# Performance work log

Hardware: AMD Instinct MI355X
Metric: run time of the kernel (lower is better)

Reference implementation:

```python
import jax, jax.numpy as jnp
import numpy as np

N_NODES = 80000
N_EDGES = 1280000
N_FEAT = 4
HIDDEN = 64
N_CLASSES = 2
N_GRAPHS = 64
BN_EPS = 1e-5


def setup_inputs() -> dict:
    key = jax.random.key(0)
    ks = jax.random.split(key, 16)
    x = jax.random.normal(ks[0], (N_NODES, N_FEAT), dtype=jnp.float32)
    edge_index = jax.random.randint(ks[1], (2, N_EDGES), 0, N_NODES, dtype=jnp.int64)
    batch = jnp.sort(jax.random.randint(ks[2], (N_NODES,), 0, N_GRAPHS, dtype=jnp.int64))

    def lin_w(k, fan_in, fan_out):
        bound = 1.0 / np.sqrt(fan_in)
        return jax.random.uniform(k, (fan_in, fan_out), jnp.float32, -bound, bound)

    inp = {
        "x": x, "edge_index": edge_index, "batch": batch,
        # BatchNorm1d (eval mode: running stats)
        "bn_gamma": jnp.ones((N_FEAT,), jnp.float32),
        "bn_beta": jnp.zeros((N_FEAT,), jnp.float32),
        "bn_mean": jnp.zeros((N_FEAT,), jnp.float32),
        "bn_var": jnp.ones((N_FEAT,), jnp.float32),
        # GraphConv layers: out = agg @ W_rel + b_rel + x @ W_root
        "W1_rel": lin_w(ks[3], N_FEAT, HIDDEN), "b1_rel": jnp.zeros((HIDDEN,), jnp.float32),
        "W1_root": lin_w(ks[4], N_FEAT, HIDDEN),
        "W2_rel": lin_w(ks[5], HIDDEN, HIDDEN), "b2_rel": jnp.zeros((HIDDEN,), jnp.float32),
        "W2_root": lin_w(ks[6], HIDDEN, HIDDEN),
        "W3_rel": lin_w(ks[7], HIDDEN, HIDDEN), "b3_rel": jnp.zeros((HIDDEN,), jnp.float32),
        "W3_root": lin_w(ks[8], HIDDEN, HIDDEN),
        "lin_W": lin_w(ks[9], HIDDEN, N_CLASSES),
        "lin_b": jnp.zeros((N_CLASSES,), jnp.float32),
    }
    return inp


def _graph_conv(x, src, dst, W_rel, b_rel, W_root):
    # PyG GraphConv: x_i' = W_root x_i + W_rel * sum_{j in N(i)} x_j + b_rel
    agg = jax.ops.segment_sum(x[src], dst, num_segments=N_NODES)  # [N, C_in]
    return agg @ W_rel + b_rel + x @ W_root


def reference(x, edge_index, batch,
              bn_gamma, bn_beta, bn_mean, bn_var,
              W1_rel, b1_rel, W1_root,
              W2_rel, b2_rel, W2_root,
              W3_rel, b3_rel, W3_root,
              lin_W, lin_b):
    src, dst = edge_index[0], edge_index[1]
    # BatchNorm1d, eval mode (running stats); dropout is a no-op in eval.
    h = (x - bn_mean) * (bn_gamma * jax.lax.rsqrt(bn_var + BN_EPS)) + bn_beta
    h = jax.nn.relu(_graph_conv(h, src, dst, W1_rel, b1_rel, W1_root))
    h = jax.nn.relu(_graph_conv(h, src, dst, W2_rel, b2_rel, W2_root))
    h = _graph_conv(h, src, dst, W3_rel, b3_rel, W3_root)
    # global mean pool over graphs
    sums = jax.ops.segment_sum(h, batch, num_segments=N_GRAPHS)        # [G, H]
    cnts = jax.ops.segment_sum(jnp.ones((h.shape[0],), h.dtype), batch,
                               num_segments=N_GRAPHS)                  # [G]
    pooled = sums / jnp.maximum(cnts, 1.0)[:, None]
    return pooled @ lin_W + lin_b  # [G, num_classes]
```

## Files before the change

kernel.cpp:

```cpp
#include <hip/hip_runtime.h>
#include <hip/hip_bf16.h>

#define N_NODES 80000
#define N_EDGES 1280000
#define N_FEAT 4
#define HIDDEN 64
#define N_GRAPHS 64
#define BN_EPS 1e-5f

#define NBUCK 313
#define BCAP 8000
#define EPT 16

typedef unsigned short ushort_t;
typedef __attribute__((ext_vector_type(8))) short bf16x8;
typedef __attribute__((ext_vector_type(4))) float f32x4;

__device__ __forceinline__ float bf2f(ushort_t v) {
    return __uint_as_float(((unsigned)v) << 16);
}
__device__ __forceinline__ ushort_t f2bf(float f) {
    unsigned u = __float_as_uint(f);
    u += 0x7FFFu + ((u >> 16) & 1u);
    return (ushort_t)(u >> 16);
}

__global__ void wprep_kernel(const float* __restrict__ W2_rel,
                             const float* __restrict__ W2_root,
                             const float* __restrict__ W3_rel,
                             const float* __restrict__ W3_root,
                             ushort_t* __restrict__ WcatT2,
                             ushort_t* __restrict__ WcatT3,
                             int* __restrict__ bcursor,
                             float* __restrict__ pool,
                             float* __restrict__ cnt) {
    int i = blockIdx.x * blockDim.x + threadIdx.x;
    int which = i >= 64 * 128;
    int j = i & (64 * 128 - 1);
    int n = j >> 7, k = j & 127;
    const float* Wr = which ? W3_rel : W2_rel;
    const float* Wo = which ? W3_root : W2_root;
    ushort_t* Wc = which ? WcatT3 : WcatT2;
    float w = (k < 64) ? Wr[k * 64 + n] : Wo[(k - 64) * 64 + n];
    Wc[j] = f2bf(w);
    if (i < 4096) pool[i] = 0.f;
    else if (i < 4160) cnt[i - 4096] = 0.f;
    else if (i < 4160 + NBUCK) bcursor[i - 4160] = 0;
}

__global__ __launch_bounds__(256) void bucket_kernel(
        const int* __restrict__ src, const int* __restrict__ dst,
        int2* __restrict__ pairs, int* __restrict__ bcursor) {
    __shared__ int hist[NBUCK];
    __shared__ int base[NBUCK];
    for (int i = threadIdx.x; i < NBUCK; i += 256) hist[i] = 0;
    __syncthreads();
    const int e0 = blockIdx.x * (256 * EPT) + threadIdx.x;
    int d[EPT], r[EPT];
#pragma unroll
    for (int k = 0; k < EPT; ++k) {
        int e = e0 + k * 256;
        if (e < N_EDGES) {
            d[k] = dst[e];
            r[k] = atomicAdd(&hist[d[k] >> 8], 1);
        }
    }
    __syncthreads();
    for (int i = threadIdx.x; i < NBUCK; i += 256) {
        int c = hist[i];
        base[i] = c ? atomicAdd(&bcursor[i], c) : 0;
    }
    __syncthreads();
#pragma unroll
    for (int k = 0; k < EPT; ++k) {
        int e = e0 + k * 256;
        if (e < N_EDGES) {
            int b = d[k] >> 8;
            int pos = base[b] + r[k];
            if (pos < BCAP) pairs[(size_t)b * BCAP + pos] = make_int2(src[e], d[k]);
        }
    }
}

__global__ __launch_bounds__(512) void bucket_scan_kernel(
        const int* __restrict__ bcursor, int* __restrict__ bbase,
        int* __restrict__ rowstart) {
    __shared__ int s[512];
    const int t = threadIdx.x;
    int v = (t < NBUCK) ? min(bcursor[t], BCAP) : 0;
    s[t] = v;
    __syncthreads();
    for (int off = 1; off < 512; off <<= 1) {
        int u = (t >= off) ? s[t - off] : 0;
        __syncthreads();
        s[t] += u;
        __syncthreads();
    }
    if (t < NBUCK) bbase[t] = s[t] - v;
    if (t == NBUCK - 1) rowstart[N_NODES] = s[t];
}

__global__ __launch_bounds__(256) void csr_build_kernel(
        const int2* __restrict__ pairs, const int* __restrict__ bcursor,
        const int* __restrict__ bbase,
        int* __restrict__ rowstart, int* __restrict__ csr) {
    __shared__ int degl[256];
    __shared__ int pref[256];
    __shared__ int curs[256];
    const int b = blockIdx.x;
    const int t = threadIdx.x;
    const int cnt = min(bcursor[b], BCAP);
    const int base = bbase[b];
    degl[t] = 0;
    __syncthreads();
    const int2* pb = pairs + (size_t)b * BCAP;
    for (int i = t; i < cnt; i += 256) {
        atomicAdd(&degl[pb[i].y & 255], 1);
    }
    __syncthreads();
    int v = degl[t];
    pref[t] = v;
    __syncthreads();
    for (int off = 1; off < 256; off <<= 1) {
        int u = (t >= off) ? pref[t - off] : 0;
        __syncthreads();
        pref[t] += u;
        __syncthreads();
    }
    int excl = pref[t] - v;
    int node = b * 256 + t;
    if (node < N_NODES) rowstart[node] = base + excl;
    curs[t] = excl;
    __syncthreads();
    for (int i = t; i < cnt; i += 256) {
        int2 p = pb[i];
        int pos = atomicAdd(&curs[p.y & 255], 1);
        csr[base + pos] = p.x;
    }
}

__global__ __launch_bounds__(1024) void layer1_kernel(
        const float* __restrict__ x, ushort_t* __restrict__ h1,
        const int* __restrict__ rowstart, const int* __restrict__ csr,
        const float* __restrict__ Wrel, const float* __restrict__ Wroot,
        const float* __restrict__ b,
        const float* __restrict__ gamma, const float* __restrict__ beta,
        const float* __restrict__ mean, const float* __restrict__ var) {
    const int lane = threadIdx.x & 63;
    const int wid = threadIdx.x >> 6;
    float scale[4], shift[4];
#pragma unroll
    for (int k = 0; k < 4; ++k) {
        float sc = gamma[k] * rsqrtf(var[k] + BN_EPS);
        scale[k] = sc;
        shift[k] = beta[k] - mean[k] * sc;
    }
    float wrel2[4], wroot2[4];
    float crel = 0.f, croot = 0.f;
#pragma unroll
    for (int k = 0; k < 4; ++k) {
        float wr = Wrel[k * 64 + lane], wo = Wroot[k * 64 + lane];
        wrel2[k] = scale[k] * wr;  crel += shift[k] * wr;
        wroot2[k] = scale[k] * wo; croot += shift[k] * wo;
    }
    const float bj = b[lane] + croot;
    const int sub = lane >> 2;
    const int f = lane & 3;
    const int nW = gridDim.x * 16;
    for (int n0 = blockIdx.x * 16 + wid; n0 < N_NODES; n0 += nW) {
        const int node = __builtin_amdgcn_readfirstlane(n0);
        const int e0 = rowstart[node], e1 = rowstart[node + 1];
        const float deg = (float)(e1 - e0);
        float part = 0.f;
        for (int e = e0 + sub; e < e1; e += 16) {
            int s = csr[e];
            part += x[s * 4 + f];
        }
        part += __shfl_xor(part, 4);
        part += __shfl_xor(part, 8);
        part += __shfl_xor(part, 16);
        part += __shfl_xor(part, 32);
        float a0 = __shfl(part, 0), a1 = __shfl(part, 1);
        float a2 = __shfl(part, 2), a3 = __shfl(part, 3);
        float x0 = x[node * 4 + 0], x1 = x[node * 4 + 1];
        float x2 = x[node * 4 + 2], x3 = x[node * 4 + 3];
        float out = bj + deg * crel
                  + a0 * wrel2[0] + a1 * wrel2[1] + a2 * wrel2[2] + a3 * wrel2[3]
                  + x0 * wroot2[0] + x1 * wroot2[1] + x2 * wroot2[2] + x3 * wroot2[3];
        h1[(size_t)node * 64 + lane] = f2bf(fmaxf(out, 0.f));
    }
}

__global__ __launch_bounds__(256) void gather_kernel(
        const ushort_t* __restrict__ hin, ushort_t* __restrict__ Gagg,
        const int* __restrict__ rowstart, const int* __restrict__ csr) {
    const int lane = threadIdx.x & 63;
    const int node = __builtin_amdgcn_readfirstlane(blockIdx.x * 4 + (threadIdx.x >> 6));
    const int e0 = rowstart[node], e1 = rowstart[node + 1];
    float a0 = 0.f, a1 = 0.f, a2 = 0.f, a3 = 0.f;
    float a4 = 0.f, a5 = 0.f, a6 = 0.f, a7 = 0.f;
    int e = e0;
    for (; e + 16 <= e1; e += 16) {
        int idx = csr[e + (lane & 15)];
        int s0 = __builtin_amdgcn_readlane(idx, 0);
        int s1 = __builtin_amdgcn_readlane(idx, 1);
        int s2 = __builtin_amdgcn_readlane(idx, 2);
        int s3 = __builtin_amdgcn_readlane(idx, 3);
        int s4 = __builtin_amdgcn_readlane(idx, 4);
        int s5 = __builtin_amdgcn_readlane(idx, 5);
        int s6 = __builtin_amdgcn_readlane(idx, 6);
        int s7 = __builtin_amdgcn_readlane(idx, 7);
        int s8 = __builtin_amdgcn_readlane(idx, 8);
        int s9 = __builtin_amdgcn_readlane(idx, 9);
        int s10 = __builtin_amdgcn_readlane(idx, 10);
        int s11 = __builtin_amdgcn_readlane(idx, 11);
        int s12 = __builtin_amdgcn_readlane(idx, 12);
        int s13 = __builtin_amdgcn_readlane(idx, 13);
        int s14 = __builtin_amdgcn_readlane(idx, 14);
        int s15 = __builtin_amdgcn_readlane(idx, 15);
        ushort_t v0 = hin[(size_t)s0 * 64 + lane];
        ushort_t v1 = hin[(size_t)s1 * 64 + lane];
        ushort_t v2 = hin[(size_t)s2 * 64 + lane];
        ushort_t v3 = hin[(size_t)s3 * 64 + lane];
        ushort_t v4 = hin[(size_t)s4 * 64 + lane];
        ushort_t v5 = hin[(size_t)s5 * 64 + lane];
        ushort_t v6 = hin[(size_t)s6 * 64 + lane];
        ushort_t v7 = hin[(size_t)s7 * 64 + lane];
        ushort_t v8 = hin[(size_t)s8 * 64 + lane];
        ushort_t v9 = hin[(size_t)s9 * 64 + lane];
        ushort_t v10 = hin[(size_t)s10 * 64 + lane];
        ushort_t v11 = hin[(size_t)s11 * 64 + lane];
        ushort_t v12 = hin[(size_t)s12 * 64 + lane];
        ushort_t v13 = hin[(size_t)s13 * 64 + lane];
        ushort_t v14 = hin[(size_t)s14 * 64 + lane];
        ushort_t v15 = hin[(size_t)s15 * 64 + lane];
        a0 += bf2f(v0) + bf2f(v8);
        a1 += bf2f(v1) + bf2f(v9);
        a2 += bf2f(v2) + bf2f(v10);
        a3 += bf2f(v3) + bf2f(v11);
        a4 += bf2f(v4) + bf2f(v12);
        a5 += bf2f(v5) + bf2f(v13);
        a6 += bf2f(v6) + bf2f(v14);
        a7 += bf2f(v7) + bf2f(v15);
    }
    if (e + 8 <= e1) {
        int idx = csr[e + (lane & 7)];
        int s0 = __builtin_amdgcn_readlane(idx, 0);
        int s1 = __builtin_amdgcn_readlane(idx, 1);
        int s2 = __builtin_amdgcn_readlane(idx, 2);
        int s3 = __builtin_amdgcn_readlane(idx, 3);
        int s4 = __builtin_amdgcn_readlane(idx, 4);
        int s5 = __builtin_amdgcn_readlane(idx, 5);
        int s6 = __builtin_amdgcn_readlane(idx, 6);
        int s7 = __builtin_amdgcn_readlane(idx, 7);
        ushort_t v0 = hin[(size_t)s0 * 64 + lane];
        ushort_t v1 = hin[(size_t)s1 * 64 + lane];
        ushort_t v2 = hin[(size_t)s2 * 64 + lane];
        ushort_t v3 = hin[(size_t)s3 * 64 + lane];
        ushort_t v4 = hin[(size_t)s4 * 64 + lane];
        ushort_t v5 = hin[(size_t)s5 * 64 + lane];
        ushort_t v6 = hin[(size_t)s6 * 64 + lane];
        ushort_t v7 = hin[(size_t)s7 * 64 + lane];
        a0 += bf2f(v0); a1 += bf2f(v1); a2 += bf2f(v2); a3 += bf2f(v3);
        a4 += bf2f(v4); a5 += bf2f(v5); a6 += bf2f(v6); a7 += bf2f(v7);
        e += 8;
    }
    if (e + 4 <= e1) {
        int idx = csr[e + (lane & 3)];
        int s0 = __builtin_amdgcn_readlane(idx, 0);
        int s1 = __builtin_amdgcn_readlane(idx, 1);
        int s2 = __builtin_amdgcn_readlane(idx, 2);
        int s3 = __builtin_amdgcn_readlane(idx, 3);
        ushort_t v0 = hin[(size_t)s0 * 64 + lane];
        ushort_t v1 = hin[(size_t)s1 * 64 + lane];
        ushort_t v2 = hin[(size_t)s2 * 64 + lane];
        ushort_t v3 = hin[(size_t)s3 * 64 + lane];
        a0 += bf2f(v0); a1 += bf2f(v1); a2 += bf2f(v2); a3 += bf2f(v3);
        e += 4;
    }
    for (; e < e1; ++e) {
        int s = __builtin_amdgcn_readfirstlane(csr[e]);
        a0 += bf2f(hin[(size_t)s * 64 + lane]);
    }
    float agg = ((a0 + a1) + (a2 + a3)) + ((a4 + a5) + (a6 + a7));
    Gagg[(size_t)node * 64 + lane] = f2bf(agg);
}

__global__ __launch_bounds__(256) void gemm_kernel(
        const ushort_t* __restrict__ Gagg, const ushort_t* __restrict__ hin,
        ushort_t* __restrict__ hout,
        const ushort_t* __restrict__ WcatT, const float* __restrict__ b,
        int relu) {
    const int lane = threadIdx.x & 63;
    const int col = lane & 15;
    const int grp = lane >> 4;

    bf16x8 bf[4][4];
#pragma unroll
    for (int kt = 0; kt < 4; ++kt)
#pragma unroll
        for (int nt = 0; nt < 4; ++nt)
            bf[kt][nt] = *(const bf16x8*)&WcatT[(nt * 16 + col) * 128 + kt * 32 + grp * 8];

    float bj[4];
#pragma unroll
    for (int nt = 0; nt < 4; ++nt) bj[nt] = b[nt * 16 + col];

    const int tile = blockIdx.x * 4 + (threadIdx.x >> 6);
    if (tile >= N_NODES / 16) return;
    const int node0 = tile * 16;

    const ushort_t* ga = Gagg + (size_t)(node0 + col) * 64 + grp * 8;
    const ushort_t* ha = hin + (size_t)(node0 + col) * 64 + grp * 8;
    f32x4 acc0 = {0.f, 0.f, 0.f, 0.f};
    f32x4 acc1 = {0.f, 0.f, 0.f, 0.f};
    f32x4 acc2 = {0.f, 0.f, 0.f, 0.f};
    f32x4 acc3 = {0.f, 0.f, 0.f, 0.f};
#pragma unroll
    for (int kt = 0; kt < 4; ++kt) {
        bf16x8 a = (kt < 2) ? *(const bf16x8*)(ga + kt * 32)
                            : *(const bf16x8*)(ha + (kt - 2) * 32);
        acc0 = __builtin_amdgcn_mfma_f32_16x16x32_bf16(a, bf[kt][0], acc0, 0, 0, 0);
        acc1 = __builtin_amdgcn_mfma_f32_16x16x32_bf16(a, bf[kt][1], acc1, 0, 0, 0);
        acc2 = __builtin_amdgcn_mfma_f32_16x16x32_bf16(a, bf[kt][2], acc2, 0, 0, 0);
        acc3 = __builtin_amdgcn_mfma_f32_16x16x32_bf16(a, bf[kt][3], acc3, 0, 0, 0);
    }

#pragma unroll
    for (int nt = 0; nt < 4; ++nt) {
        f32x4 acc = (nt == 0) ? acc0 : (nt == 1) ? acc1 : (nt == 2) ? acc2 : acc3;
        const int c = nt * 16 + col;
#pragma unroll
        for (int r = 0; r < 4; ++r) {
            int row = grp * 4 + r;
            float v = acc[r] + bj[nt];
            if (relu) v = fmaxf(v, 0.f);
            hout[(size_t)(node0 + row) * 64 + c] = f2bf(v);
        }
    }
}

__global__ void pool_kernel(const ushort_t* __restrict__ h3, const int* __restrict__ batch,
                            float* __restrict__ pool, float* __restrict__ cnt) {
    const int lane = threadIdx.x & 63;
    const int gw = (blockIdx.x * blockDim.x + threadIdx.x) >> 6;
    const int nW = (gridDim.x * blockDim.x) >> 6;
    const int chunk = (N_NODES + nW - 1) / nW;
    int n0 = gw * chunk;
    int n1 = n0 + chunk; if (n1 > N_NODES) n1 = N_NODES;
    if (n0 >= N_NODES) return;
    float acc = 0.f;
    int cur = batch[n0];
    int cl = 0;
#define POOL_FLUSH() do { atomicAdd(&pool[cur * 64 + lane], acc); \
        if (lane == 0) atomicAdd(&cnt[cur], (float)cl); acc = 0.f; cl = 0; } while (0)
    int n = n0;
    for (; n + 8 <= n1; n += 8) {
        float v0 = bf2f(h3[(size_t)(n + 0) * 64 + lane]);
        float v1 = bf2f(h3[(size_t)(n + 1) * 64 + lane]);
        float v2 = bf2f(h3[(size_t)(n + 2) * 64 + lane]);
        float v3 = bf2f(h3[(size_t)(n + 3) * 64 + lane]);
        float v4 = bf2f(h3[(size_t)(n + 4) * 64 + lane]);
        float v5 = bf2f(h3[(size_t)(n + 5) * 64 + lane]);
        float v6 = bf2f(h3[(size_t)(n + 6) * 64 + lane]);
        float v7 = bf2f(h3[(size_t)(n + 7) * 64 + lane]);
        int g0 = batch[n + 0], g1 = batch[n + 1], g2 = batch[n + 2], g3 = batch[n + 3];
        int g4 = batch[n + 4], g5 = batch[n + 5], g6 = batch[n + 6], g7 = batch[n + 7];
        if (g0 != cur) { POOL_FLUSH(); cur = g0; } acc += v0; cl++;
        if (g1 != cur) { POOL_FLUSH(); cur = g1; } acc += v1; cl++;
        if (g2 != cur) { POOL_FLUSH(); cur = g2; } acc += v2; cl++;
        if (g3 != cur) { POOL_FLUSH(); cur = g3; } acc += v3; cl++;
        if (g4 != cur) { POOL_FLUSH(); cur = g4; } acc += v4; cl++;
        if (g5 != cur) { POOL_FLUSH(); cur = g5; } acc += v5; cl++;
        if (g6 != cur) { POOL_FLUSH(); cur = g6; } acc += v6; cl++;
        if (g7 != cur) { POOL_FLUSH(); cur = g7; } acc += v7; cl++;
    }
    for (; n < n1; ++n) {
        int g = batch[n];
        if (g != cur) { POOL_FLUSH(); cur = g; }
        acc += bf2f(h3[(size_t)n * 64 + lane]);
        cl++;
    }
    atomicAdd(&pool[cur * 64 + lane], acc);
    if (lane == 0) atomicAdd(&cnt[cur], (float)cl);
#undef POOL_FLUSH
}

__global__ void head_kernel(const float* __restrict__ pool, const float* __restrict__ cnt,
                            const float* __restrict__ linW, const float* __restrict__ linb,
                            float* __restrict__ out) {
    int g = threadIdx.x >> 1;
    int c = threadIdx.x & 1;
    if (g < N_GRAPHS) {
        float inv = 1.0f / fmaxf(cnt[g], 1.0f);
        float acc = linb[c];
        for (int j = 0; j < 64; ++j) acc += pool[g * 64 + j] * inv * linW[j * 2 + c];
        out[g * 2 + c] = acc;
    }
}

extern "C" void kernel_launch(void* const* d_in, const int* in_sizes, int n_in,
                              void* d_out, int out_size, void* d_ws, size_t ws_size,
                              hipStream_t stream) {
    const float* x = (const float*)d_in[0];
    const int* edge_index = (const int*)d_in[1];
    const int* batch = (const int*)d_in[2];
    const float* bn_gamma = (const float*)d_in[3];
    const float* bn_beta = (const float*)d_in[4];
    const float* bn_mean = (const float*)d_in[5];
    const float* bn_var = (const float*)d_in[6];
    const float* W1_rel = (const float*)d_in[7];
    const float* b1_rel = (const float*)d_in[8];
    const float* W1_root = (const float*)d_in[9];
    const float* W2_rel = (const float*)d_in[10];
    const float* b2_rel = (const float*)d_in[11];
    const float* W2_root = (const float*)d_in[12];
    const float* W3_rel = (const float*)d_in[13];
    const float* b3_rel = (const float*)d_in[14];
    const float* W3_root = (const float*)d_in[15];
    const float* lin_W = (const float*)d_in[16];
    const float* lin_b = (const float*)d_in[17];
    float* out = (float*)d_out;

    const int* e_src = edge_index;
    const int* e_dst = edge_index + N_EDGES;

    ushort_t* h1 = (ushort_t*)d_ws;
    ushort_t* h2 = h1 + 5120000;
    float* pool = (float*)(h2 + 5120000);
    float* cnt = pool + 4096;
    int* bcursor = (int*)(cnt + 64);
    int* bbase = bcursor + 320;
    int* rowstart = bbase + 320;
    int* csr = rowstart + 80016;
    ushort_t* WcatT2 = (ushort_t*)(csr + 1280000);
    ushort_t* WcatT3 = WcatT2 + 8192;
    ushort_t* Gagg = (ushort_t*)(WcatT3 + 8192 + 16);
    int2* pairs = (int2*)h1;
    ushort_t* h3 = h1;

    wprep_kernel<<<64, 256, 0, stream>>>(W2_rel, W2_root, W3_rel, W3_root,
                                         WcatT2, WcatT3, bcursor, pool, cnt);

    bucket_kernel<<<(N_EDGES + 256 * EPT - 1) / (256 * EPT), 256, 0, stream>>>(
        e_src, e_dst, pairs, bcursor);
    bucket_scan_kernel<<<1, 512, 0, stream>>>(bcursor, bbase, rowstart);
    csr_build_kernel<<<NBUCK, 256, 0, stream>>>(pairs, bcursor, bbase, rowstart, csr);

    layer1_kernel<<<512, 1024, 0, stream>>>(x, h1, rowstart, csr, W1_rel, W1_root,
                                            b1_rel, bn_gamma, bn_beta, bn_mean, bn_var);

    gather_kernel<<<N_NODES / 4, 256, 0, stream>>>(h1, Gagg, rowstart, csr);
    gemm_kernel<<<N_NODES / 64, 256, 0, stream>>>(Gagg, h1, h2, WcatT2, b2_rel, 1);

    gather_kernel<<<N_NODES / 4, 256, 0, stream>>>(h2, Gagg, rowstart, csr);
    gemm_kernel<<<N_NODES / 64, 256, 0, stream>>>(Gagg, h2, h3, WcatT3, b3_rel, 0);

    pool_kernel<<<256, 256, 0, stream>>>(h3, batch, pool, cnt);
    head_kernel<<<1, 128, 0, stream>>>(pool, cnt, lin_W, lin_b, out);
}
```

Before: 175.9 us.

## Pack edge pairs to 32 bits, fold bucket scan into CSR build, fuse pool+head

Edge pairs are packed into one 32-bit word (17-bit source, 8-bit local destination) instead of an int2, halving the bucket write and read traffic. The separate single-block bucket scan is removed: each CSR-build block recomputes its own base with a block reduction over the preceding bucket counts. The pooling and head kernels are merged, with the last block to finish (tracked by an atomic counter) computing the final linear layer. Together this drops two kernel launches at the cost of redundant prefix sums and a global completion counter.

Measured after the change: 182.9 us. 4.0% more time.

```diff
diff --git a/kernel.cpp b/kernel.cpp
--- a/kernel.cpp
+++ b/kernel.cpp
@@ -33,7 +33,8 @@
                              ushort_t* __restrict__ WcatT3,
                              int* __restrict__ bcursor,
                              float* __restrict__ pool,
-                             float* __restrict__ cnt) {
+                             float* __restrict__ cnt,
+                             int* __restrict__ done) {
     int i = blockIdx.x * blockDim.x + threadIdx.x;
     int which = i >= 64 * 128;
     int j = i & (64 * 128 - 1);
@@ -46,11 +47,12 @@
     if (i < 4096) pool[i] = 0.f;
     else if (i < 4160) cnt[i - 4096] = 0.f;
     else if (i < 4160 + NBUCK) bcursor[i - 4160] = 0;
+    else if (i == 4160 + NBUCK) *done = 0;
 }
 
 __global__ __launch_bounds__(256) void bucket_kernel(
         const int* __restrict__ src, const int* __restrict__ dst,
-        int2* __restrict__ pairs, int* __restrict__ bcursor) {
+        unsigned* __restrict__ pairs, int* __restrict__ bcursor) {
     __shared__ int hist[NBUCK];
     __shared__ int base[NBUCK];
     for (int i = threadIdx.x; i < NBUCK; i += 256) hist[i] = 0;
@@ -77,45 +79,37 @@
         if (e < N_EDGES) {
             int b = d[k] >> 8;
             int pos = base[b] + r[k];
-            if (pos < BCAP) pairs[(size_t)b * BCAP + pos] = make_int2(src[e], d[k]);
-        }
-    }
-}
-
-__global__ __launch_bounds__(512) void bucket_scan_kernel(
-        const int* __restrict__ bcursor, int* __restrict__ bbase,
-        int* __restrict__ rowstart) {
-    __shared__ int s[512];
-    const int t = threadIdx.x;
-    int v = (t < NBUCK) ? min(bcursor[t], BCAP) : 0;
-    s[t] = v;
-    __syncthreads();
-    for (int off = 1; off < 512; off <<= 1) {
-        int u = (t >= off) ? s[t - off] : 0;
-        __syncthreads();
-        s[t] += u;
-        __syncthreads();
-    }
-    if (t < NBUCK) bbase[t] = s[t] - v;
-    if (t == NBUCK - 1) rowstart[N_NODES] = s[t];
+            if (pos < BCAP)
+                pairs[(size_t)b * BCAP + pos] =
+                    (unsigned)src[e] | (((unsigned)d[k] & 255u) << 17);
+        }
+    }
 }
 
 __global__ __launch_bounds__(256) void csr_build_kernel(
-        const int2* __restrict__ pairs, const int* __restrict__ bcursor,
-        const int* __restrict__ bbase,
+        const unsigned* __restrict__ pairs, const int* __restrict__ bcursor,
         int* __restrict__ rowstart, int* __restrict__ csr) {
     __shared__ int degl[256];
     __shared__ int pref[256];
     __shared__ int curs[256];
     const int b = blockIdx.x;
     const int t = threadIdx.x;
-    const int cnt = min(bcursor[b], BCAP);
-    const int base = bbase[b];
+    int partial = 0;
+    for (int i = t; i < b; i += 256) partial += min(bcursor[i], BCAP);
+    pref[t] = partial;
+    __syncthreads();
+    for (int off = 128; off > 0; off >>= 1) {
+        if (t < off) pref[t] += pref[t + off];
+        __syncthreads();
+    }
+    const int base = pref[0];
+    const int cntb = min(bcursor[b], BCAP);
+    __syncthreads();
     degl[t] = 0;
     __syncthreads();
-    const int2* pb = pairs + (size_t)b * BCAP;
-    for (int i = t; i < cnt; i += 256) {
-        atomicAdd(&degl[pb[i].y & 255], 1);
+    const unsigned* pb = pairs + (size_t)b * BCAP;
+    for (int i = t; i < cntb; i += 256) {
+        atomicAdd(&degl[pb[i] >> 17], 1);
     }
     __syncthreads();
     int v = degl[t];
@@ -130,12 +124,13 @@
     int excl = pref[t] - v;
     int node = b * 256 + t;
     if (node < N_NODES) rowstart[node] = base + excl;
+    if (b == NBUCK - 1 && t == 255) rowstart[N_NODES] = base + cntb;
     curs[t] = excl;
     __syncthreads();
-    for (int i = t; i < cnt; i += 256) {
-        int2 p = pb[i];
-        int pos = atomicAdd(&curs[p.y & 255], 1);
-        csr[base + pos] = p.x;
+    for (int i = t; i < cntb; i += 256) {
+        unsigned p = pb[i];
+        int pos = atomicAdd(&curs[p >> 17], 1);
+        csr[base + pos] = (int)(p & 0x1FFFFu);
     }
 }
 
@@ -340,62 +335,72 @@
     }
 }
 
-__global__ void pool_kernel(const ushort_t* __restrict__ h3, const int* __restrict__ batch,
-                            float* __restrict__ pool, float* __restrict__ cnt) {
+__global__ __launch_bounds__(256) void pool_head_kernel(
+        const ushort_t* __restrict__ h3, const int* __restrict__ batch,
+        float* __restrict__ pool, float* __restrict__ cnt, int* __restrict__ done,
+        const float* __restrict__ linW, const float* __restrict__ linb,
+        float* __restrict__ out) {
     const int lane = threadIdx.x & 63;
     const int gw = (blockIdx.x * blockDim.x + threadIdx.x) >> 6;
     const int nW = (gridDim.x * blockDim.x) >> 6;
     const int chunk = (N_NODES + nW - 1) / nW;
     int n0 = gw * chunk;
     int n1 = n0 + chunk; if (n1 > N_NODES) n1 = N_NODES;
-    if (n0 >= N_NODES) return;
-    float acc = 0.f;
-    int cur = batch[n0];
-    int cl = 0;
+    if (n0 < N_NODES) {
+        float acc = 0.f;
+        int cur = batch[n0];
+        int cl = 0;
 #define POOL_FLUSH() do { atomicAdd(&pool[cur * 64 + lane], acc); \
         if (lane == 0) atomicAdd(&cnt[cur], (float)cl); acc = 0.f; cl = 0; } while (0)
-    int n = n0;
-    for (; n + 8 <= n1; n += 8) {
-        float v0 = bf2f(h3[(size_t)(n + 0) * 64 + lane]);
-        float v1 = bf2f(h3[(size_t)(n + 1) * 64 + lane]);
-        float v2 = bf2f(h3[(size_t)(n + 2) * 64 + lane]);
-        float v3 = bf2f(h3[(size_t)(n + 3) * 64 + lane]);
-        float v4 = bf2f(h3[(size_t)(n + 4) * 64 + lane]);
-        float v5 = bf2f(h3[(size_t)(n + 5) * 64 + lane]);
-        float v6 = bf2f(h3[(size_t)(n + 6) * 64 + lane]);
-        float v7 = bf2f(h3[(size_t)(n + 7) * 64 + lane]);
-        int g0 = batch[n + 0], g1 = batch[n + 1], g2 = batch[n + 2], g3 = batch[n + 3];
-        int g4 = batch[n + 4], g5 = batch[n + 5], g6 = batch[n + 6], g7 = batch[n + 7];
-        if (g0 != cur) { POOL_FLUSH(); cur = g0; } acc += v0; cl++;
-        if (g1 != cur) { POOL_FLUSH(); cur = g1; } acc += v1; cl++;
-        if (g2 != cur) { POOL_FLUSH(); cur = g2; } acc += v2; cl++;
-        if (g3 != cur) { POOL_FLUSH(); cur = g3; } acc += v3; cl++;
-        if (g4 != cur) { POOL_FLUSH(); cur = g4; } acc += v4; cl++;
-        if (g5 != cur) { POOL_FLUSH(); cur = g5; } acc += v5; cl++;
-        if (g6 != cur) { POOL_FLUSH(); cur = g6; } acc += v6; cl++;
-        if (g7 != cur) { POOL_FLUSH(); cur = g7; } acc += v7; cl++;
-    }
-    for (; n < n1; ++n) {
-        int g = batch[n];
-        if (g != cur) { POOL_FLUSH(); cur = g; }
-        acc += bf2f(h3[(size_t)n * 64 + lane]);
-        cl++;
-    }
-    atomicAdd(&pool[cur * 64 + lane], acc);
-    if (lane == 0) atomicAdd(&cnt[cur], (float)cl);
+        int n = n0;
+        for (; n + 8 <= n1; n += 8) {
+            float v0 = bf2f(h3[(size_t)(n + 0) * 64 + lane]);
+            float v1 = bf2f(h3[(size_t)(n + 1) * 64 + lane]);
+            float v2 = bf2f(h3[(size_t)(n + 2) * 64 + lane]);
+            float v3 = bf2f(h3[(size_t)(n + 3) * 64 + lane]);
+            float v4 = bf2f(h3[(size_t)(n + 4) * 64 + lane]);
+            float v5 = bf2f(h3[(size_t)(n + 5) * 64 + lane]);
+            float v6 = bf2f(h3[(size_t)(n + 6) * 64 + lane]);
+            float v7 = bf2f(h3[(size_t)(n + 7) * 64 + lane]);
+            int g0 = batch[n + 0], g1 = batch[n + 1], g2 = batch[n + 2], g3 = batch[n + 3];
+            int g4 = batch[n + 4], g5 = batch[n + 5], g6 = batch[n + 6], g7 = batch[n + 7];
+            if (g0 != cur) { POOL_FLUSH(); cur = g0; } acc += v0; cl++;
+            if (g1 != cur) { POOL_FLUSH(); cur = g1; } acc += v1; cl++;
+            if (g2 != cur) { POOL_FLUSH(); cur = g2; } acc += v2; cl++;
+            if (g3 != cur) { POOL_FLUSH(); cur = g3; } acc += v3; cl++;
+            if (g4 != cur) { POOL_FLUSH(); cur = g4; } acc += v4; cl++;
+            if (g5 != cur) { POOL_FLUSH(); cur = g5; } acc += v5; cl++;
+            if (g6 != cur) { POOL_FLUSH(); cur = g6; } acc += v6; cl++;
+            if (g7 != cur) { POOL_FLUSH(); cur = g7; } acc += v7; cl++;
+        }
+        for (; n < n1; ++n) {
+            int g = batch[n];
+            if (g != cur) { POOL_FLUSH(); cur = g; }
+            acc += bf2f(h3[(size_t)n * 64 + lane]);
+            cl++;
+        }
+        atomicAdd(&pool[cur * 64 + lane], acc);
+        if (lane == 0) atomicAdd(&cnt[cur], (float)cl);
 #undef POOL_FLUSH
-}
-
-__global__ void head_kernel(const float* __restrict__ pool, const float* __restrict__ cnt,
-                            const float* __restrict__ linW, const float* __restrict__ linb,
-                            float* __restrict__ out) {
-    int g = threadIdx.x >> 1;
-    int c = threadIdx.x & 1;
-    if (g < N_GRAPHS) {
-        float inv = 1.0f / fmaxf(cnt[g], 1.0f);
-        float acc = linb[c];
-        for (int j = 0; j < 64; ++j) acc += pool[g * 64 + j] * inv * linW[j * 2 + c];
-        out[g * 2 + c] = acc;
+    }
+    __threadfence();
+    __syncthreads();
+    __shared__ int lastFlag;
+    if (threadIdx.x == 0) {
+        int t = atomicAdd(done, 1);
+        lastFlag = (t == (int)gridDim.x - 1);
+    }
+    __syncthreads();
+    if (lastFlag) {
+        __threadfence();
+        int g = threadIdx.x >> 1;
+        int c = threadIdx.x & 1;
+        if (threadIdx.x < 128) {
+            float inv = 1.0f / fmaxf(cnt[g], 1.0f);
+            float acc = linb[c];
+            for (int j = 0; j < 64; ++j) acc += pool[g * 64 + j] * inv * linW[j * 2 + c];
+            out[g * 2 + c] = acc;
+        }
     }
 }
 
@@ -430,22 +435,21 @@
     float* pool = (float*)(h2 + 5120000);
     float* cnt = pool + 4096;
     int* bcursor = (int*)(cnt + 64);
-    int* bbase = bcursor + 320;
-    int* rowstart = bbase + 320;
+    int* done = bcursor + 316;
+    int* rowstart = bcursor + 320 + 320;
     int* csr = rowstart + 80016;
     ushort_t* WcatT2 = (ushort_t*)(csr + 1280000);
     ushort_t* WcatT3 = WcatT2 + 8192;
     ushort_t* Gagg = (ushort_t*)(WcatT3 + 8192 + 16);
-    int2* pairs = (int2*)h1;
+    unsigned* pairs = (unsigned*)h1;
     ushort_t* h3 = h1;
 
     wprep_kernel<<<64, 256, 0, stream>>>(W2_rel, W2_root, W3_rel, W3_root,
-                                         WcatT2, WcatT3, bcursor, pool, cnt);
+                                         WcatT2, WcatT3, bcursor, pool, cnt, done);
 
     bucket_kernel<<<(N_EDGES + 256 * EPT - 1) / (256 * EPT), 256, 0, stream>>>(
         e_src, e_dst, pairs, bcursor);
-    bucket_scan_kernel<<<1, 512, 0, stream>>>(bcursor, bbase, rowstart);
-    csr_build_kernel<<<NBUCK, 256, 0, stream>>>(pairs, bcursor, bbase, rowstart, csr);
+    csr_build_kernel<<<NBUCK, 256, 0, stream>>>(pairs, bcursor, rowstart, csr);
 
     layer1_kernel<<<512, 1024, 0, stream>>>(x, h1, rowstart, csr, W1_rel, W1_root,
                                             b1_rel, bn_gamma, bn_beta, bn_mean, bn_var);
@@ -456,6 +460,6 @@
     gather_kernel<<<N_NODES / 4, 256, 0, stream>>>(h2, Gagg, rowstart, csr);
     gemm_kernel<<<N_NODES / 64, 256, 0, stream>>>(Gagg, h2, h3, WcatT3, b3_rel, 0);
 
-    pool_kernel<<<256, 256, 0, stream>>>(h3, batch, pool, cnt);
-    head_kernel<<<1, 128, 0, stream>>>(pool, cnt, lin_W, lin_b, out);
-}
+    pool_head_kernel<<<256, 256, 0, stream>>>(h3, batch, pool, cnt, done,
+                                              lin_W, lin_b, out);
+}
```
